# Kernel tuning notes

Hardware: AMD Instinct MI355X
Metric: run time of the kernel (lower is better)

The kernel has to match this reference:

```python
import jax, jax.numpy as jnp
import numpy as np

HEADS = 24
HEAD_DIM = 96
SPARSE_N = 4
ROPE_FREQ = 10000.0


def _rope_axis(x, pos, scale):
    # x: (s, b, h, D) with D even; pos: (s,) integer positions along one axis
    D = x.shape[-1]
    inv_freq = 1.0 / (ROPE_FREQ ** (jnp.arange(0, D, 2, dtype=jnp.float32) / D))
    t = pos.astype(jnp.float32) / scale
    freqs = t[:, None] * inv_freq[None, :]            # (s, D/2)
    emb = jnp.concatenate([freqs, freqs], axis=-1)    # (s, D)
    cos = jnp.cos(emb)[:, None, None, :]              # broadcast over (b, h)
    sin = jnp.sin(emb)[:, None, None, :]
    x1, x2 = jnp.split(x, 2, axis=-1)
    rot = jnp.concatenate([-x2, x1], axis=-1)         # rotate_half
    return x * cos + rot * sin


def _rope3d(x, frame, height, width, scales=(1.0, 1.0, 1.0)):
    # x: (s, b, h, d); head dim is split into 3 equal chunks for t/h/w axes
    s, b, h, d = x.shape
    D = d // 3
    tt, hh, ww = jnp.meshgrid(jnp.arange(frame), jnp.arange(height), jnp.arange(width), indexing='ij')
    pos_t, pos_h, pos_w = tt.reshape(-1), hh.reshape(-1), ww.reshape(-1)
    return jnp.concatenate([
        _rope_axis(x[..., :D], pos_t, scales[0]),
        _rope_axis(x[..., D:2 * D], pos_h, scales[1]),
        _rope_axis(x[..., 2 * D:], pos_w, scales[2]),
    ], axis=-1)


def setup_inputs() -> dict:
    key = jax.random.key(0)
    ks = jax.random.split(key, 9)
    frame, height, width, b = 8, 16, 16, 4
    s = frame * height * width          # 2048
    dim = HEADS * HEAD_DIM              # 2304
    w_scale = 0.02
    return {
        'hidden_states': jax.random.normal(ks[0], (s, b, dim), jnp.float32),
        'wq': jax.random.normal(ks[1], (dim, dim), jnp.float32) * w_scale,
        'bq': jnp.zeros((dim,), jnp.float32),
        'wk': jax.random.normal(ks[2], (dim, dim), jnp.float32) * w_scale,
        'bk': jnp.zeros((dim,), jnp.float32),
        'wv': jax.random.normal(ks[3], (dim, dim), jnp.float32) * w_scale,
        'bv': jnp.zeros((dim,), jnp.float32),
        'wo': jax.random.normal(ks[4], (dim, dim), jnp.float32) * w_scale,
        'bo': jnp.zeros((dim,), jnp.float32),
        'frame': frame,
        'height': height,
        'width': width,
    }


def reference(hidden_states, wq, bq, wk, bk, wv, bv, wo, bo, frame, height, width):
    # hidden_states: (s, b, dim) in SBH layout, self-attention path (no seq-parallel)
    s, b, dim = hidden_states.shape
    n = SPARSE_N

    q = hidden_states @ wq + bq
    k = hidden_states @ wk + bk
    v = hidden_states @ wv + bv

    # 3D RoPE on q/k, per-head
    q = _rope3d(q.reshape(s, b, HEADS, HEAD_DIM), frame, height, width).reshape(s, b, dim)
    k = _rope3d(k.reshape(s, b, HEADS, HEAD_DIM), frame, height, width).reshape(s, b, dim)

    # _sparse_1d (sparse_group=False): pad s to multiple of n*n, then
    # '(g k) b d -> g (k b) d' == contiguous reshape
    pad_len = (-s) % (n * n)
    sp_s = (s + pad_len) // n
    sp_b = n * b

    def sparse(x):
        if pad_len:
            x = jnp.pad(x, ((0, pad_len), (0, 0), (0, 0)))
        return x.reshape(sp_s, sp_b, dim)

    q, k, v = sparse(q), sparse(k), sparse(v)

    # 's b (h d) -> b h s d'
    def to_bhsd(x):
        return x.reshape(sp_s, sp_b, HEADS, HEAD_DIM).transpose(1, 2, 0, 3)

    qh, kh, vh = to_bhsd(q), to_bhsd(k), to_bhsd(v)

    # scaled dot-product attention (no mask, no dropout, non-causal)
    scale = HEAD_DIM ** -0.5
    scores = jnp.einsum('bhqd,bhkd->bhqk', qh, kh) * scale
    attn = jax.nn.softmax(scores, axis=-1)
    out = jnp.einsum('bhqk,bhkd->bhqd', attn, vh)

    # 'b h s d -> s b (h d)', reverse sparse rearrange, drop padding
    out = out.transpose(2, 0, 1, 3).reshape(sp_s, sp_b, dim)
    out = out.reshape(sp_s * n, b, dim)[:s]

    # to_out[0] linear, to_out[1] dropout (identity in eval), rescale_output_factor=1
    return out @ wo + bo
```

## Files before the change

kernel.cpp:

```cpp
#include <hip/hip_runtime.h>
#include <hip/hip_bf16.h>

typedef __attribute__((ext_vector_type(8))) __bf16 bf16x8;
typedef __attribute__((ext_vector_type(4))) __bf16 bf16x4;
typedef __attribute__((ext_vector_type(4))) float  f32x4;

#define DIM   2304
#define NH    24
#define HD    96
#define SPS   512

__device__ __forceinline__ void gload16(const void* gp, void* lp) {
  __builtin_amdgcn_global_load_lds(
      (__attribute__((address_space(1))) void*)(unsigned long long)gp,
      (__attribute__((address_space(3))) void*)lp, 16, 0, 0);
}

__global__ __launch_bounds__(256) void prep_kernel(
    const float* __restrict__ hs,
    const float* __restrict__ wq, const float* __restrict__ wk,
    const float* __restrict__ wv, const float* __restrict__ wo,
    __bf16* __restrict__ hsb, __bf16* __restrict__ wqkvT, __bf16* __restrict__ woT)
{
  __shared__ float t[64][65];
  const int bid = blockIdx.x;
  const int tid = threadIdx.x;
  if (bid < 5184) {
    const int z = bid / 1296;
    const int rest = bid - z * 1296;
    const int n0 = (rest % 36) * 64, k0 = (rest / 36) * 64;
    const float* src = (z == 0) ? wq : (z == 1) ? wk : (z == 2) ? wv : wo;
    __bf16* dst = (z < 3) ? (wqkvT + (size_t)z * DIM * DIM) : woT;
    const int tx = tid & 63, ty = tid >> 6;
#pragma unroll
    for (int j = 0; j < 64; j += 4)
      t[ty + j][tx] = src[(size_t)(k0 + ty + j) * DIM + n0 + tx];
    __syncthreads();
#pragma unroll
    for (int j = 0; j < 64; j += 4)
      dst[(size_t)(n0 + ty + j) * DIM + k0 + tx] = (__bf16)t[tx][ty + j];
  } else {
    const int i = (bid - 5184) * 256 + tid;
    const float4 f = ((const float4*)hs)[i];
    bf16x4 o = { (__bf16)f.x, (__bf16)f.y, (__bf16)f.z, (__bf16)f.w };
    ((bf16x4*)hsb)[i] = o;
  }
}


template<int NJ>
__device__ __forceinline__ void stage_half(
    const __bf16* __restrict__ X, __bf16* lX, int r0, int k0,
    int srow, int schunk, int dslot)
{
#pragma unroll
  for (int j = 0; j < NJ; ++j)
    gload16(X + (size_t)(r0 + j * 64 + srow) * DIM + k0 + schunk,
            lX + (j * 64 + srow) * 64 + dslot);
}

template<int MF, int H, int Q, bool LA, bool LB>
__device__ __forceinline__ void phase8(
    const char* ab, const char* bb, int wm, int wn, int laneA0, int laneA1,
    bf16x8 (&a)[MF][2], bf16x8 (&bq)[2][2][2], f32x4 (&acc)[2 * MF][4])
{
  if (LA) {
#pragma unroll
    for (int fm = 0; fm < MF; ++fm) {
      a[fm][0] = *(const bf16x8*)(ab + (wm * (MF * 32) + H * (MF * 16) + fm * 16) * 128 + laneA0);
      a[fm][1] = *(const bf16x8*)(ab + (wm * (MF * 32) + H * (MF * 16) + fm * 16) * 128 + laneA1);
    }
  }
  if (LB) {
#pragma unroll
    for (int fn = 0; fn < 2; ++fn) {
      bq[Q][fn][0] = *(const bf16x8*)(bb + (wn * 64 + Q * 32 + fn * 16) * 128 + laneA0);
      bq[Q][fn][1] = *(const bf16x8*)(bb + (wn * 64 + Q * 32 + fn * 16) * 128 + laneA1);
    }
  }
  __builtin_amdgcn_s_barrier();
  asm volatile("s_waitcnt lgkmcnt(0)" ::: "memory");
  __builtin_amdgcn_s_setprio(1);
#pragma unroll
  for (int fm = 0; fm < MF; ++fm)
#pragma unroll
    for (int fn = 0; fn < 2; ++fn)
#pragma unroll
      for (int kk = 0; kk < 2; ++kk)
        acc[H * MF + fm][Q * 2 + fn] = __builtin_amdgcn_mfma_f32_16x16x32_bf16(
            a[fm][kk], bq[Q][fn][kk], acc[H * MF + fm][Q * 2 + fn], 0, 0, 0);
  __builtin_amdgcn_s_setprio(0);
  __builtin_amdgcn_s_barrier();
}

template<int EPI, int MF, int GRID>
__global__ __launch_bounds__(512, 2) void gemm8p_kernel(
    const __bf16* __restrict__ A, const __bf16* __restrict__ B,
    const float* __restrict__ b0, const float* __restrict__ b1, const float* __restrict__ b2,
    __bf16* __restrict__ o0, __bf16* __restrict__ o1, __bf16* __restrict__ o2,
    float* __restrict__ fout)
{
  constexpr int MROWS = MF * 64;
  constexpr int VG = MF + 4;
  __shared__ __align__(16) __bf16 As[2][MROWS * 64];
  __shared__ __align__(16) __bf16 Bs[2][256 * 64];
  __shared__ float tcos[640], tsin[640];
  const int tid = threadIdx.x;
  if (EPI == 0) {
    for (int i = tid; i < 640; i += 512) {
      int pos, jj = i & 15;
      if (i < 128)      pos = i >> 4;
      else if (i < 384) pos = (i - 128) >> 4;
      else              pos = (i - 384) >> 4;
      const float invf = exp2f(-(float)jj * 0.83048202372184059f);
      float s, c;
      sincosf((float)pos * invf, &s, &c);
      tcos[i] = c; tsin[i] = s;
    }
  }
  const int wid = tid >> 6, l = tid & 63;
  const int lq = l & 15, lg = l >> 4;
  const int wm = wid >> 2, wn = wid & 3;
  const int bid = blockIdx.x;
  const int xcd = bid & 7, local = bid >> 3;
  int m0, n0;
  if (GRID == 0) {
    m0 = (xcd * 4 + (local & 3)) * 256;
    n0 = (local >> 2) * 256;
  } else if (GRID == 1) {
    m0 = (xcd * 4 + ((local >> 1) & 3)) * 256 + (local & 1) * 128;
    n0 = (24 + (local >> 3)) * 256;
  } else if (GRID == 2) {
    m0 = (xcd * 8 + (local & 7)) * 128;
    n0 = (local >> 3) * 256;
  } else {
    m0 = (xcd * 8 + (local >> 1)) * 128 + (local & 1) * 64;
    n0 = 2048;
  }
  const int srow = tid >> 3;
  const int schunk = ((tid & 7) ^ (srow & 7)) * 8;
  const int dslot = (tid & 7) * 8;
  const int laneA0 = lq * 128 + ((lg * 16) ^ ((lq & 7) << 4));
  const int laneA1 = lq * 128 + ((64 + lg * 16) ^ ((lq & 7) << 4));

  f32x4 acc[2 * MF][4] = {};
  bf16x8 a[MF][2], bq[2][2][2];

  stage_half<MF>(A, As[0], m0, 0, srow, schunk, dslot);
  stage_half<4>(B, Bs[0], n0, 0, srow, schunk, dslot);
  stage_half<MF>(A, As[1], m0, 64, srow, schunk, dslot);
  stage_half<4>(B, Bs[1], n0, 64, srow, schunk, dslot);
  asm volatile("s_waitcnt vmcnt(%0)" :: "n"(VG) : "memory");
  __builtin_amdgcn_s_barrier();

  const char* a0p = (const char*)&As[0][0];
  const char* b0p = (const char*)&Bs[0][0];
  const char* a1p = (const char*)&As[1][0];
  const char* b1p = (const char*)&Bs[1][0];

#define TILE_STAGED(AP, BP, SA, SB, KN)                                          \
  phase8<MF, 0, 0, true,  true >(AP, BP, wm, wn, laneA0, laneA1, a, bq, acc);    \
  phase8<MF, 0, 1, false, true >(AP, BP, wm, wn, laneA0, laneA1, a, bq, acc);    \
  stage_half<4>(B, SB, n0, KN, srow, schunk, dslot);                             \
  phase8<MF, 1, 1, true,  false>(AP, BP, wm, wn, laneA0, laneA1, a, bq, acc);    \
  stage_half<MF>(A, SA, m0, KN, srow, schunk, dslot);                            \
  phase8<MF, 1, 0, false, false>(AP, BP, wm, wn, laneA0, laneA1, a, bq, acc);    \
  asm volatile("s_waitcnt vmcnt(%0)" :: "n"(VG) : "memory");                     \
  __builtin_amdgcn_s_barrier();

#define TILE_PLAIN(AP, BP)                                                       \
  phase8<MF, 0, 0, true,  true >(AP, BP, wm, wn, laneA0, laneA1, a, bq, acc);    \
  phase8<MF, 0, 1, false, true >(AP, BP, wm, wn, laneA0, laneA1, a, bq, acc);    \
  phase8<MF, 1, 1, true,  false>(AP, BP, wm, wn, laneA0, laneA1, a, bq, acc);    \
  phase8<MF, 1, 0, false, false>(AP, BP, wm, wn, laneA0, laneA1, a, bq, acc);

  for (int tt = 0; tt < 34; tt += 2) {
    TILE_STAGED(a0p, b0p, As[0], Bs[0], (tt + 2) * 64)
    TILE_STAGED(a1p, b1p, As[1], Bs[1], (tt + 3) * 64)
  }
  TILE_PLAIN(a0p, b0p)
  asm volatile("s_waitcnt vmcnt(0)" ::: "memory");
  __builtin_amdgcn_s_barrier();
  TILE_PLAIN(a1p, b1p)
#undef TILE_STAGED
#undef TILE_PLAIN

  if (EPI == 0) {
    const int mat = n0 / DIM;
    const int nb = n0 - mat * DIM;
    const float* bias = (mat == 0) ? b0 : (mat == 1) ? b1 : b2;
    __bf16* outp = (mat == 0) ? o0 : (mat == 1) ? o1 : o2;
#pragma unroll
    for (int mr = 0; mr < 2 * MF; ++mr) {
      const int gq = (m0 + wm * (MF * 32) + mr * 16) >> 4;
      const int si = gq * 4 + lg;
      const int pos3[3] = { si >> 8, (si >> 4) & 15, si & 15 };
#pragma unroll
      for (int p = 0; p < 2; ++p) {
        const int nlo = nb + wn * 64 + (2 * p) * 16 + lq;
        const int nhi = nlo + 16;
        const int hlo = nlo / HD, dlo = nlo - hlo * HD;
        const int hhi = nhi / HD, dhi = nhi - hhi * HD;
        const float blo = bias[nlo], bhi = bias[nhi];
        float c = 1.f, s = 0.f;
        if (mat < 2) {
          const int cix = dlo >> 5;
          const int toff = ((cix == 0) ? 0 : (cix == 1) ? 128 : 384) + pos3[cix] * 16 + lq;
          c = tcos[toff]; s = tsin[toff];
        }
#pragma unroll
        for (int r = 0; r < 4; ++r) {
          const int bp = lg * 4 + r;
          const float x1 = acc[mr][2 * p][r] + blo;
          const float x2 = acc[mr][2 * p + 1][r] + bhi;
          float y1 = x1, y2 = x2;
          if (mat < 2) { y1 = x1 * c - x2 * s; y2 = x2 * c + x1 * s; }
          outp[((size_t)(bp * NH + hlo) * SPS + gq) * HD + dlo] = (__bf16)y1;
          outp[((size_t)(bp * NH + hhi) * SPS + gq) * HD + dhi] = (__bf16)y2;
        }
      }
    }
  } else {
#pragma unroll
    for (int mr = 0; mr < 2 * MF; ++mr) {
      const int rbase = m0 + wm * (MF * 32) + mr * 16;
#pragma unroll
      for (int nr = 0; nr < 4; ++nr) {
        const int n = n0 + wn * 64 + nr * 16 + lq;
        const float bia = b0[n];
#pragma unroll
        for (int r = 0; r < 4; ++r)
          fout[(size_t)(rbase + lg * 4 + r) * DIM + n] = acc[mr][nr][r] + bia;
      }
    }
  }
}

__global__ __launch_bounds__(256) void transpose_v_kernel(
    const __bf16* __restrict__ v, __bf16* __restrict__ vT)
{
  __shared__ __bf16 t[96][72];
  const int tid = threadIdx.x, bid = blockIdx.x;
  const int bh = bid >> 3, g0 = (bid & 7) * 64;
  const __bf16* src = v + ((size_t)bh * SPS + g0) * HD;
#pragma unroll
  for (int it = 0; it < 3; ++it) {
    const int lin = it * 256 + tid;
    const int row = lin / 12, c8 = (lin % 12) * 8;
    bf16x8 x = *(const bf16x8*)(src + row * HD + c8);
#pragma unroll
    for (int j = 0; j < 8; ++j) {
      const int d = c8 + j;
      t[d][row ^ ((d & 7) << 3)] = x[j];
    }
  }
  __syncthreads();
  __bf16* dst = vT + (size_t)bh * HD * SPS + g0;
#pragma unroll
  for (int it = 0; it < 3; ++it) {
    const int lin = it * 256 + tid;
    const int d = lin / 8, gc = (lin % 8) * 8;
    bf16x8 o = *(const bf16x8*)&t[d][gc ^ ((d & 7) << 3)];
    *(bf16x8*)(dst + (size_t)d * SPS + (gc ^ ((d & 7) << 3))) = o;
  }
}

__global__ __launch_bounds__(256) void attn_kernel(
    const __bf16* __restrict__ q, const __bf16* __restrict__ k,
    const __bf16* __restrict__ vTs, __bf16* __restrict__ ao)
{
  __shared__ __align__(16) __bf16 Vt[2][96 * 64];
  __shared__ __bf16 Pl[4][16 * 72];
  const int tid = threadIdx.x;
  const int w = tid >> 6, l = tid & 63;
  const int lq = l & 15, lg = l >> 4;
  const int bid = blockIdx.x;
  const int swz = (bid & 7) * 384 + (bid >> 3);
  const int qt = swz & 7;
  const int h  = (swz >> 3) % NH;
  const int bp = swz / (NH * 8);
  const size_t bh = (size_t)bp * NH + h;
  const __bf16* qb = q + bh * SPS * HD;
  const __bf16* kb = k + bh * SPS * HD;
  const __bf16* vb = vTs + bh * HD * SPS;
  const int vrow = w * 24 + (l >> 3);
  const int vcol = (l & 7) * 8;
  bf16x8 qf[3];
  {
    const __bf16* qr = qb + (size_t)(qt * 64 + w * 16 + lq) * HD + lg * 8;
    qf[0] = *(const bf16x8*)(qr);
    qf[1] = *(const bf16x8*)(qr + 32);
    qf[2] = *(const bf16x8*)(qr + 64);
  }
  const float sc = 0.10206207261596575f * 1.4426950408889634f;
  float m_run = -1e30f, l_run = 0.f;
  f32x4 o[6] = {};
#pragma unroll
  for (int j = 0; j < 3; ++j)
    gload16(vb + (size_t)(vrow + j * 8) * SPS + vcol,
            &Vt[0][(vrow + j * 8) * 64 + vcol]);

  for (int t = 0; t < 8; ++t) {
    const int cur = t & 1;
    const int kb0 = t * 64;
    __builtin_amdgcn_s_barrier();
    f32x4 st[4];
    __builtin_amdgcn_s_setprio(1);
#pragma unroll
    for (int t2 = 0; t2 < 4; ++t2) {
      const __bf16* kr = kb + (size_t)(kb0 + t2 * 16 + lq) * HD + lg * 8;
      bf16x8 k0f = *(const bf16x8*)(kr);
      bf16x8 k1f = *(const bf16x8*)(kr + 32);
      bf16x8 k2f = *(const bf16x8*)(kr + 64);
      f32x4 s = {};
      s = __builtin_amdgcn_mfma_f32_16x16x32_bf16(k0f, qf[0], s, 0, 0, 0);
      s = __builtin_amdgcn_mfma_f32_16x16x32_bf16(k1f, qf[1], s, 0, 0, 0);
      s = __builtin_amdgcn_mfma_f32_16x16x32_bf16(k2f, qf[2], s, 0, 0, 0);
      st[t2] = s;
    }
    __builtin_amdgcn_s_setprio(0);
    __builtin_amdgcn_sched_barrier(0);
    if (t < 7) {
#pragma unroll
      for (int j = 0; j < 3; ++j)
        gload16(vb + (size_t)(vrow + j * 8) * SPS + (kb0 + 64) + vcol,
                &Vt[1 - cur][(vrow + j * 8) * 64 + vcol]);
    }
    __builtin_amdgcn_sched_barrier(0);
    float pmax = -1e30f;
#pragma unroll
    for (int t2 = 0; t2 < 4; ++t2)
#pragma unroll
      for (int r = 0; r < 4; ++r) pmax = fmaxf(pmax, st[t2][r]);
    pmax *= sc;
    if (__any(pmax > m_run + 8.f)) {
      float mn = fmaxf(m_run, pmax);
      mn = fmaxf(mn, __shfl_xor(mn, 16));
      mn = fmaxf(mn, __shfl_xor(mn, 32));
      const float alpha = exp2f(m_run - mn);
      l_run *= alpha;
      float al[4];
#pragma unroll
      for (int r = 0; r < 4; ++r) al[r] = __shfl(alpha, lg * 4 + r);
#pragma unroll
      for (int ni = 0; ni < 6; ++ni)
#pragma unroll
        for (int r = 0; r < 4; ++r) o[ni][r] *= al[r];
      m_run = mn;
    }
#pragma unroll
    for (int t2 = 0; t2 < 4; ++t2) {
      bf16x4 pb;
#pragma unroll
      for (int r = 0; r < 4; ++r) {
        const float p = exp2f(st[t2][r] * sc - m_run);
        l_run += p;
        pb[r] = (__bf16)p;
      }
      *(bf16x4*)&Pl[w][lq * 72 + t2 * 16 + lg * 4] = pb;
    }
    if (t < 7) { asm volatile("s_waitcnt vmcnt(3)" ::: "memory"); }
    else       { asm volatile("s_waitcnt vmcnt(0)" ::: "memory"); }
    __builtin_amdgcn_s_barrier();
#pragma unroll
    for (int ks = 0; ks < 2; ++ks) {
      bf16x8 pa = *(const bf16x8*)&Pl[w][lq * 72 + ks * 32 + lg * 8];
      __builtin_amdgcn_s_setprio(1);
#pragma unroll
      for (int ni = 0; ni < 6; ++ni) {
        const int col = (ks * 32 + lg * 8) ^ ((lq & 7) << 3);
        bf16x8 vf = *(const bf16x8*)&Vt[cur][(ni * 16 + lq) * 64 + col];
        o[ni] = __builtin_amdgcn_mfma_f32_16x16x32_bf16(pa, vf, o[ni], 0, 0, 0);
      }
      __builtin_amdgcn_s_setprio(0);
    }
  }
  l_run += __shfl_xor(l_run, 16);
  l_run += __shfl_xor(l_run, 32);
  float linv[4];
#pragma unroll
  for (int r = 0; r < 4; ++r) linv[r] = 1.f / __shfl(l_run, lg * 4 + r);
#pragma unroll
  for (int ni = 0; ni < 6; ++ni)
#pragma unroll
    for (int r = 0; r < 4; ++r) {
      const int gq = qt * 64 + w * 16 + lg * 4 + r;
      const int d = ni * 16 + lq;
      ao[(size_t)(gq * 16 + bp) * DIM + h * HD + d] = (__bf16)(o[ni][r] * linv[r]);
    }
}

extern "C" void kernel_launch(void* const* d_in, const int* in_sizes, int n_in,
                              void* d_out, int out_size, void* d_ws, size_t ws_size,
                              hipStream_t stream) {
  const float* hs = (const float*)d_in[0];
  const float* wq = (const float*)d_in[1];
  const float* bq = (const float*)d_in[2];
  const float* wk = (const float*)d_in[3];
  const float* bk = (const float*)d_in[4];
  const float* wv = (const float*)d_in[5];
  const float* bv = (const float*)d_in[6];
  const float* wo = (const float*)d_in[7];
  const float* bo = (const float*)d_in[8];
  float* out = (float*)d_out;

  char* ws = (char*)d_ws;
  __bf16* wqkvT = (__bf16*)(ws);
  __bf16* hsb   = (__bf16*)(ws + 31850496);
  __bf16* qb    = (__bf16*)(ws + 69599232);
  __bf16* kbuf  = (__bf16*)(ws + 107347968);
  __bf16* vbuf  = (__bf16*)(ws + 145096704);
  __bf16* woT   = (__bf16*)(ws + 182845440);
  __bf16* vbufT = (__bf16*)(ws);
  __bf16* ao    = vbuf;

  prep_kernel<<<23616, 256, 0, stream>>>(hs, wq, wk, wv, wo, hsb, wqkvT, woT);
  gemm8p_kernel<0, 4, 0><<<768, 512, 0, stream>>>(hsb, wqkvT, bq, bk, bv, qb, kbuf, vbuf, nullptr);
  gemm8p_kernel<0, 2, 1><<<192, 512, 0, stream>>>(hsb, wqkvT, bq, bk, bv, qb, kbuf, vbuf, nullptr);
  transpose_v_kernel<<<3072, 256, 0, stream>>>(vbuf, vbufT);
  attn_kernel<<<3072, 256, 0, stream>>>(qb, kbuf, vbufT, ao);
  gemm8p_kernel<1, 2, 2><<<512, 512, 0, stream>>>(ao, woT, bo, nullptr, nullptr, nullptr, nullptr, nullptr, out);
  gemm8p_kernel<1, 1, 3><<<128, 512, 0, stream>>>(ao, woT, bo, nullptr, nullptr, nullptr, nullptr, nullptr, out);
}
```

Measured before the change: 512.0 us.

## Stage K tiles through LDS in attention and restructure GEMM phase loads

New measurement: 492.1 us. 1.04x faster.

```diff
diff --git a/kernel.cpp b/kernel.cpp
--- a/kernel.cpp
+++ b/kernel.cpp
@@ -57,40 +57,6 @@
   for (int j = 0; j < NJ; ++j)
     gload16(X + (size_t)(r0 + j * 64 + srow) * DIM + k0 + schunk,
             lX + (j * 64 + srow) * 64 + dslot);
-}
-
-template<int MF, int H, int Q, bool LA, bool LB>
-__device__ __forceinline__ void phase8(
-    const char* ab, const char* bb, int wm, int wn, int laneA0, int laneA1,
-    bf16x8 (&a)[MF][2], bf16x8 (&bq)[2][2][2], f32x4 (&acc)[2 * MF][4])
-{
-  if (LA) {
-#pragma unroll
-    for (int fm = 0; fm < MF; ++fm) {
-      a[fm][0] = *(const bf16x8*)(ab + (wm * (MF * 32) + H * (MF * 16) + fm * 16) * 128 + laneA0);
-      a[fm][1] = *(const bf16x8*)(ab + (wm * (MF * 32) + H * (MF * 16) + fm * 16) * 128 + laneA1);
-    }
-  }
-  if (LB) {
-#pragma unroll
-    for (int fn = 0; fn < 2; ++fn) {
-      bq[Q][fn][0] = *(const bf16x8*)(bb + (wn * 64 + Q * 32 + fn * 16) * 128 + laneA0);
-      bq[Q][fn][1] = *(const bf16x8*)(bb + (wn * 64 + Q * 32 + fn * 16) * 128 + laneA1);
-    }
-  }
-  __builtin_amdgcn_s_barrier();
-  asm volatile("s_waitcnt lgkmcnt(0)" ::: "memory");
-  __builtin_amdgcn_s_setprio(1);
-#pragma unroll
-  for (int fm = 0; fm < MF; ++fm)
-#pragma unroll
-    for (int fn = 0; fn < 2; ++fn)
-#pragma unroll
-      for (int kk = 0; kk < 2; ++kk)
-        acc[H * MF + fm][Q * 2 + fn] = __builtin_amdgcn_mfma_f32_16x16x32_bf16(
-            a[fm][kk], bq[Q][fn][kk], acc[H * MF + fm][Q * 2 + fn], 0, 0, 0);
-  __builtin_amdgcn_s_setprio(0);
-  __builtin_amdgcn_s_barrier();
 }
 
 template<int EPI, int MF, int GRID>
@@ -144,7 +110,25 @@
   const int laneA1 = lq * 128 + ((64 + lg * 16) ^ ((lq & 7) << 4));
 
   f32x4 acc[2 * MF][4] = {};
-  bf16x8 a[MF][2], bq[2][2][2];
+  bf16x8 a[MF][2], b0r[2][2], b1r[2][2];
+
+#define LOAD_A(APx, Hh) do { _Pragma("unroll")                                   \
+  for (int fm = 0; fm < MF; ++fm) {                                              \
+    a[fm][0] = *(const bf16x8*)((APx) + (wm * (MF * 32) + (Hh) * (MF * 16) + fm * 16) * 128 + laneA0); \
+    a[fm][1] = *(const bf16x8*)((APx) + (wm * (MF * 32) + (Hh) * (MF * 16) + fm * 16) * 128 + laneA1); } } while (0)
+
+#define LOAD_B(dst, BPx, Qq) do { _Pragma("unroll")                              \
+  for (int fn = 0; fn < 2; ++fn) {                                               \
+    dst[fn][0] = *(const bf16x8*)((BPx) + (wn * 64 + (Qq) * 32 + fn * 16) * 128 + laneA0); \
+    dst[fn][1] = *(const bf16x8*)((BPx) + (wn * 64 + (Qq) * 32 + fn * 16) * 128 + laneA1); } } while (0)
+
+#define MFMA_C(bset, Hh, Qq) do { __builtin_amdgcn_s_setprio(1); _Pragma("unroll") \
+  for (int fm = 0; fm < MF; ++fm) _Pragma("unroll")                              \
+    for (int fn = 0; fn < 2; ++fn) _Pragma("unroll")                             \
+      for (int kk = 0; kk < 2; ++kk)                                             \
+        acc[(Hh) * MF + fm][(Qq) * 2 + fn] = __builtin_amdgcn_mfma_f32_16x16x32_bf16( \
+            a[fm][kk], bset[fn][kk], acc[(Hh) * MF + fm][(Qq) * 2 + fn], 0, 0, 0); \
+  __builtin_amdgcn_s_setprio(0); } while (0)
 
   stage_half<MF>(A, As[0], m0, 0, srow, schunk, dslot);
   stage_half<4>(B, Bs[0], n0, 0, srow, schunk, dslot);
@@ -159,20 +143,32 @@
   const char* b1p = (const char*)&Bs[1][0];
 
 #define TILE_STAGED(AP, BP, SA, SB, KN)                                          \
-  phase8<MF, 0, 0, true,  true >(AP, BP, wm, wn, laneA0, laneA1, a, bq, acc);    \
-  phase8<MF, 0, 1, false, true >(AP, BP, wm, wn, laneA0, laneA1, a, bq, acc);    \
+  LOAD_A(AP, 0); LOAD_B(b0r, BP, 0); LOAD_B(b1r, BP, 1);                         \
+  __builtin_amdgcn_s_barrier();                                                  \
+  MFMA_C(b0r, 0, 0);                                                             \
+  __builtin_amdgcn_s_barrier();                                                  \
+  MFMA_C(b1r, 0, 1);                                                             \
+  LOAD_A(AP, 1);                                                                 \
+  __builtin_amdgcn_s_barrier();                                                  \
   stage_half<4>(B, SB, n0, KN, srow, schunk, dslot);                             \
-  phase8<MF, 1, 1, true,  false>(AP, BP, wm, wn, laneA0, laneA1, a, bq, acc);    \
+  MFMA_C(b1r, 1, 1);                                                             \
+  __builtin_amdgcn_s_barrier();                                                  \
   stage_half<MF>(A, SA, m0, KN, srow, schunk, dslot);                            \
-  phase8<MF, 1, 0, false, false>(AP, BP, wm, wn, laneA0, laneA1, a, bq, acc);    \
+  MFMA_C(b0r, 1, 0);                                                             \
   asm volatile("s_waitcnt vmcnt(%0)" :: "n"(VG) : "memory");                     \
   __builtin_amdgcn_s_barrier();
 
 #define TILE_PLAIN(AP, BP)                                                       \
-  phase8<MF, 0, 0, true,  true >(AP, BP, wm, wn, laneA0, laneA1, a, bq, acc);    \
-  phase8<MF, 0, 1, false, true >(AP, BP, wm, wn, laneA0, laneA1, a, bq, acc);    \
-  phase8<MF, 1, 1, true,  false>(AP, BP, wm, wn, laneA0, laneA1, a, bq, acc);    \
-  phase8<MF, 1, 0, false, false>(AP, BP, wm, wn, laneA0, laneA1, a, bq, acc);
+  LOAD_A(AP, 0); LOAD_B(b0r, BP, 0); LOAD_B(b1r, BP, 1);                         \
+  __builtin_amdgcn_s_barrier();                                                  \
+  MFMA_C(b0r, 0, 0);                                                             \
+  __builtin_amdgcn_s_barrier();                                                  \
+  MFMA_C(b1r, 0, 1);                                                             \
+  LOAD_A(AP, 1);                                                                 \
+  __builtin_amdgcn_s_barrier();                                                  \
+  MFMA_C(b1r, 1, 1);                                                             \
+  __builtin_amdgcn_s_barrier();                                                  \
+  MFMA_C(b0r, 1, 0);
 
   for (int tt = 0; tt < 34; tt += 2) {
     TILE_STAGED(a0p, b0p, As[0], Bs[0], (tt + 2) * 64)
@@ -184,6 +180,9 @@
   TILE_PLAIN(a1p, b1p)
 #undef TILE_STAGED
 #undef TILE_PLAIN
+#undef LOAD_A
+#undef LOAD_B
+#undef MFMA_C
 
   if (EPI == 0) {
     const int mat = n0 / DIM;
@@ -269,6 +268,7 @@
     const __bf16* __restrict__ q, const __bf16* __restrict__ k,
     const __bf16* __restrict__ vTs, __bf16* __restrict__ ao)
 {
+  __shared__ __align__(16) __bf16 Kt[2][64 * 96];
   __shared__ __align__(16) __bf16 Vt[2][96 * 64];
   __shared__ __bf16 Pl[4][16 * 72];
   const int tid = threadIdx.x;
@@ -281,7 +281,7 @@
   const int bp = swz / (NH * 8);
   const size_t bh = (size_t)bp * NH + h;
   const __bf16* qb = q + bh * SPS * HD;
-  const __bf16* kb = k + bh * SPS * HD;
+  const char* kbytes = (const char*)(k + bh * SPS * HD);
   const __bf16* vb = vTs + bh * HD * SPS;
   const int vrow = w * 24 + (l >> 3);
   const int vcol = (l & 7) * 8;
@@ -297,6 +297,9 @@
   f32x4 o[6] = {};
 #pragma unroll
   for (int j = 0; j < 3; ++j)
+    gload16(kbytes + j * 4096 + tid * 16, (char*)&Kt[0][0] + j * 4096 + tid * 16);
+#pragma unroll
+  for (int j = 0; j < 3; ++j)
     gload16(vb + (size_t)(vrow + j * 8) * SPS + vcol,
             &Vt[0][(vrow + j * 8) * 64 + vcol]);
 
@@ -304,11 +307,25 @@
     const int cur = t & 1;
     const int kb0 = t * 64;
     __builtin_amdgcn_s_barrier();
+    if (t < 7) {
+#pragma unroll
+      for (int j = 0; j < 3; ++j)
+        gload16(kbytes + (size_t)(kb0 + 64) * 192 + j * 4096 + tid * 16,
+                (char*)&Kt[1 - cur][0] + j * 4096 + tid * 16);
+#pragma unroll
+      for (int j = 0; j < 3; ++j)
+        gload16(vb + (size_t)(vrow + j * 8) * SPS + (kb0 + 64) + vcol,
+                &Vt[1 - cur][(vrow + j * 8) * 64 + vcol]);
+      asm volatile("s_waitcnt vmcnt(6)" ::: "memory");
+    } else {
+      asm volatile("s_waitcnt vmcnt(0)" ::: "memory");
+    }
+    __builtin_amdgcn_s_barrier();
     f32x4 st[4];
     __builtin_amdgcn_s_setprio(1);
 #pragma unroll
     for (int t2 = 0; t2 < 4; ++t2) {
-      const __bf16* kr = kb + (size_t)(kb0 + t2 * 16 + lq) * HD + lg * 8;
+      const __bf16* kr = &Kt[cur][(t2 * 16 + lq) * 96 + lg * 8];
       bf16x8 k0f = *(const bf16x8*)(kr);
       bf16x8 k1f = *(const bf16x8*)(kr + 32);
       bf16x8 k2f = *(const bf16x8*)(kr + 64);
@@ -319,14 +336,6 @@
       st[t2] = s;
     }
     __builtin_amdgcn_s_setprio(0);
-    __builtin_amdgcn_sched_barrier(0);
-    if (t < 7) {
-#pragma unroll
-      for (int j = 0; j < 3; ++j)
-        gload16(vb + (size_t)(vrow + j * 8) * SPS + (kb0 + 64) + vcol,
-                &Vt[1 - cur][(vrow + j * 8) * 64 + vcol]);
-    }
-    __builtin_amdgcn_sched_barrier(0);
     float pmax = -1e30f;
 #pragma unroll
     for (int t2 = 0; t2 < 4; ++t2)
@@ -359,9 +368,6 @@
       }
       *(bf16x4*)&Pl[w][lq * 72 + t2 * 16 + lg * 4] = pb;
     }
-    if (t < 7) { asm volatile("s_waitcnt vmcnt(3)" ::: "memory"); }
-    else       { asm volatile("s_waitcnt vmcnt(0)" ::: "memory"); }
-    __builtin_amdgcn_s_barrier();
 #pragma unroll
     for (int ks = 0; ks < 2; ++ks) {
       bf16x8 pa = *(const bf16x8*)&Pl[w][lq * 72 + ks * 32 + lg * 8];
```
